# Kernel optimization log

Measured on AMD Instinct MI355X. Metric: run time of the kernel, lower is better.

## Reference

```python
import jax, jax.numpy as jnp
import numpy as np

B, L, V, D, H = 4096, 32, 50000, 300, 6
HD = D // H  # 50


def setup_inputs() -> dict:
    key = jax.random.key(0)
    ks = jax.random.split(key, 9)
    s = 0.02
    return {
        "title": jax.random.randint(ks[0], (B, L), 0, V),
        "emb": jax.random.normal(ks[1], (V, D), dtype=jnp.float32) * s,
        "pos_emb": jax.random.normal(ks[2], (512, D), dtype=jnp.float32) * s,
        "Wq": jax.random.normal(ks[3], (D, D), dtype=jnp.float32) * s,
        "bq": jnp.zeros((D,), jnp.float32),
        "Wk": jax.random.normal(ks[4], (D, D), dtype=jnp.float32) * s,
        "bk": jnp.zeros((D,), jnp.float32),
        "Wv": jax.random.normal(ks[5], (D, D), dtype=jnp.float32) * s,
        "bv": jnp.zeros((D,), jnp.float32),
        "Wo": jax.random.normal(ks[6], (D, D), dtype=jnp.float32) * s,
        "bo": jnp.zeros((D,), jnp.float32),
        "Va": jax.random.normal(ks[7], (D, D), dtype=jnp.float32) * s,
        "ba": jnp.zeros((D,), jnp.float32),
        "qw": jax.random.normal(ks[8], (D, 1), dtype=jnp.float32) * s,
    }


def reference(title, emb, pos_emb, Wq, bq, Wk, bk, Wv, bv, Wo, bo, Va, ba, qw):
    b, l = title.shape
    # word embedding + positional embedding
    x = emb[title] + pos_emb[:l][None, :, :]  # [B, L, D]

    def heads(y):  # [B, L, D] -> [B, H, L, HD]
        return y.reshape(b, l, H, HD).transpose(0, 2, 1, 3)

    # manual multi-head self-attention (mask is all-ones -> no masking effect)
    q = heads(x @ Wq.T + bq) / jnp.sqrt(jnp.float32(HD))
    k = heads(x @ Wk.T + bk)
    v = heads(x @ Wv.T + bv)
    scores = jnp.einsum("bhqd,bhkd->bhqk", q, k)  # [B, H, L, L]
    w = jax.nn.softmax(scores, axis=-1)  # dropout is identity in eval
    ctx = jnp.einsum("bhqk,bhkd->bhqd", w, v)
    ctx = ctx.transpose(0, 2, 1, 3).reshape(b, l, D)
    ctx = ctx @ Wo.T + bo  # [B, L, D]

    # additive attention pooling
    t = jnp.tanh(ctx @ Va.T + ba)          # [B, L, D]
    a = (t @ qw)[..., 0]                    # [B, L]
    alpha = jax.nn.softmax(a, axis=1)       # [B, L]
    out = jnp.einsum("bs,bsd->bd", alpha, ctx)  # [B, D]
    return out
```

## Files before the change

### kernel.cpp

```cpp
#include <hip/hip_runtime.h>
#include <math.h>

typedef _Float16 f16;
typedef _Float16 half8 __attribute__((ext_vector_type(8)));
typedef _Float16 half4 __attribute__((ext_vector_type(4)));
typedef float float4v __attribute__((ext_vector_type(4)));

#define MFMA16(a, b, c) __builtin_amdgcn_mfma_f32_16x16x32_f16((a), (b), (c), 0, 0, 0)


#define WQKV_OFF 0u
#define BQKV_OFF 655360u
#define WO_OFF   659456u
#define WVA_OFF  864256u
#define BVA_OFF  1069056u
#define CBAR_OFF 1070336u
#define XF_OFF   3691776u

__global__ void repack1(const float* __restrict__ Wq, const float* __restrict__ Wk,
                        const float* __restrict__ Wv, const float* __restrict__ Wo,
                        const float* __restrict__ bq, const float* __restrict__ bk,
                        const float* __restrict__ bv,
                        f16* __restrict__ wqkvF, f16* __restrict__ wo16F,
                        float* __restrict__ bqkv) {
    int idx = blockIdx.x * 256 + threadIdx.x;
    const float rs = 0.14142135623730951f;
    if (idx < 327680) {
        int ntile = idx / 5120, rem = idx - ntile * 5120;
        int ks = rem / 512, r2 = rem - ks * 512;
        int lane = r2 >> 3, j = r2 & 7;
        int n = ntile * 16 + (lane & 15);
        int k = ks * 32 + (lane >> 4) * 8 + j;
        int g = n / 320, r = n - g * 320;
        float v = 0.f;
        if (r < 300 && k < 300) {
            if (g == 0) v = Wq[r * 300 + k] * rs;
            else if (g == 1) v = Wk[r * 300 + k];
            else if (g == 2) v = Wv[r * 300 + k];
        }
        wqkvF[idx] = (f16)v;
    } else if (idx < 430080) {
        int t = idx - 327680;
        int ntile = t / 5120, rem = t - ntile * 5120;
        int ks = rem / 512, r2 = rem - ks * 512;
        int lane = r2 >> 3, j = r2 & 7;
        int n = ntile * 16 + (lane & 15);
        int k = ks * 32 + (lane >> 4) * 8 + j;
        wo16F[t] = (f16)((n < 300 && k < 300) ? Wo[n * 300 + k] : 0.f);
    } else if (idx < 431104) {
        int n = idx - 430080;
        int g = n / 320, r = n - g * 320;
        float v = 0.f;
        if (r < 300) {
            if (g == 0) v = bq[r] * rs;
            else if (g == 1) v = bk[r];
            else if (g == 2) v = bv[r];
        }
        bqkv[n] = v;
    }
}

__global__ void repack2(const float* __restrict__ Va, const float* __restrict__ Wo,
                        f16* __restrict__ wvaF) {
    int bt = blockIdx.x;
    int mt = bt / 20, nt = bt % 20;
    int lane = threadIdx.x & 63;
    int lr = lane & 15, quad = lane >> 4;
    float4v acc = {0.f, 0.f, 0.f, 0.f};
    int m = mt * 16 + lr;
    int nn = nt * 16 + lr;
    for (int ks = 0; ks < 10; ++ks) {
        int c = ks * 32 + quad * 8;
        half8 af, bf;
#pragma unroll
        for (int j = 0; j < 8; ++j) {
            int cc = c + j;
            af[j] = (f16)((m < 300 && cc < 300) ? Va[m * 300 + cc] : 0.f);
            bf[j] = (f16)((nn < 300 && cc < 300) ? Wo[cc * 300 + nn] : 0.f);
        }
        acc = MFMA16(af, bf, acc);
    }
#pragma unroll
    for (int r = 0; r < 4; ++r) {
        int row = mt * 16 + quad * 4 + r;
        int col = nt * 16 + lr;
        int addr = ((row >> 4) * 10 + (col >> 5)) * 512 +
                   (((col >> 3) & 3) * 16 + (row & 15)) * 8 + (col & 7);
        wvaF[addr] = (f16)acc[r];
    }
}

__global__ void repack3(const float* __restrict__ Va, const float* __restrict__ bo,
                        const float* __restrict__ ba, float* __restrict__ bva) {
    int j = threadIdx.x;
    float s = 0.f;
    if (j < 300) {
        for (int k = 0; k < 300; ++k) s += Va[j * 300 + k] * bo[k];
        s += ba[j];
    }
    bva[j] = s;
}

__global__ void gather_kernel(const int* __restrict__ title, const float* __restrict__ emb,
                              const float* __restrict__ pos, f16* __restrict__ xF) {
    int c = blockIdx.x * 256 + threadIdx.x;
    int fragblk = c >> 6, lane = c & 63;
    int item = fragblk / 20, rem = fragblk - item * 20;
    int mt = rem / 10, ks = rem - mt * 10;
    int lr = lane & 15, quad = lane >> 4;
    int row = item * 32 + mt * 16 + lr;
    int col = ks * 32 + quad * 8;
    int t = title[row];
    int l = row & 31;
    half8 h;
    if (col + 8 <= 300) {
        float4v e0 = *(const float4v*)&emb[t * 300 + col];
        float4v e1 = *(const float4v*)&emb[t * 300 + col + 4];
        float4v p0 = *(const float4v*)&pos[l * 300 + col];
        float4v p1 = *(const float4v*)&pos[l * 300 + col + 4];
#pragma unroll
        for (int j = 0; j < 4; ++j) { h[j] = (f16)(e0[j] + p0[j]); h[4 + j] = (f16)(e1[j] + p1[j]); }
    } else {
#pragma unroll
        for (int j = 0; j < 8; ++j) {
            int cc = col + j;
            h[j] = (f16)((cc < 300) ? emb[t * 300 + cc] + pos[l * 300 + cc] : 0.f);
        }
    }
    *(half8*)&xF[c * 8] = h;
}

__global__ __launch_bounds__(1024, 4) void qkvattn_kernel(
    const f16* __restrict__ xF, const f16* __restrict__ wqkvF,
    const float* __restrict__ bqkv, const f16* __restrict__ wvaF,
    const float* __restrict__ bva, const float* __restrict__ qw,
    f16* __restrict__ cbar) {
    __shared__ __align__(16) f16 qL[12 * 32 * 72];
    __shared__ __align__(16) f16 kL[12 * 32 * 72];
    __shared__ __align__(16) f16 vT[12 * 64 * 32];
    __shared__ float aL[64];
    __shared__ float alpha[64];
    const int ib = blockIdx.x, tid = threadIdx.x;
    const int w = tid >> 6, lane = tid & 63, lr = lane & 15, quad = lane >> 4;
    const float4v vz = {0.f, 0.f, 0.f, 0.f};

    for (int i = tid; i < 13824; i += 1024) { ((int*)qL)[i] = 0; ((int*)kL)[i] = 0; }
    for (int i = tid; i < 12288; i += 1024) ((int*)vT)[i] = 0;
    if (tid < 64) aL[tid] = 0.f;
    __syncthreads();

    {
        float4v acc[4][4];
#pragma unroll
        for (int mt = 0; mt < 4; ++mt)
#pragma unroll
            for (int j = 0; j < 4; ++j) acc[mt][j] = vz;
        for (int ks = 0; ks < 10; ++ks) {
            half8 a[4];
#pragma unroll
            for (int mt = 0; mt < 4; ++mt)
                a[mt] = *(const half8*)&xF[(((ib * 4 + mt) * 10 + ks) * 64 + lane) * 8];
#pragma unroll
            for (int j = 0; j < 4; ++j) {
                half8 bf = *(const half8*)&wqkvF[((((w * 4 + j) * 10) + ks) * 64 + lane) * 8];
#pragma unroll
                for (int mt = 0; mt < 4; ++mt) acc[mt][j] = MFMA16(a[mt], bf, acc[mt][j]);
            }
        }
#pragma unroll
        for (int j = 0; j < 4; ++j) {
            int tile = w * 4 + j;
            int wi = tile / 20;
            int n = tile * 16 + lr;
            int cc = n - wi * 320;
            float bb = (wi < 3) ? bqkv[n] : 0.f;
            int h = cc / 50, d = cc - h * 50;
            if (wi < 3 && cc < 300) {
                if (wi == 2) {
#pragma unroll
                    for (int mt = 0; mt < 4; ++mt) {
                        int hh = (mt >> 1) * 6 + h;
                        int row0 = (mt & 1) * 16 + quad * 4;
                        half4 pk;
#pragma unroll
                        for (int r = 0; r < 4; ++r) pk[r] = (f16)(acc[mt][j][r] + bb);
                        *(half4*)&vT[(hh * 64 + d) * 32 + row0] = pk;
                    }
                } else {
                    f16* dst = (wi == 0) ? qL : kL;
#pragma unroll
                    for (int mt = 0; mt < 4; ++mt) {
                        int hh = (mt >> 1) * 6 + h;
#pragma unroll
                        for (int r = 0; r < 4; ++r) {
                            int row = (mt & 1) * 16 + quad * 4 + r;
                            dst[(hh * 32 + row) * 72 + d] = (f16)(acc[mt][j][r] + bb);
                        }
                    }
                }
            }
        }
    }
    __syncthreads();

    const int hh = w;
    if (w < 12) {
        float4v s00 = vz, s01 = vz, s10 = vz, s11 = vz;
#pragma unroll
        for (int ks = 0; ks < 2; ++ks) {
            int c = ks * 32 + quad * 8;
            half8 aq0 = *(const half8*)&qL[(hh * 32 + lr) * 72 + c];
            half8 aq1 = *(const half8*)&qL[(hh * 32 + 16 + lr) * 72 + c];
            half8 bk0 = *(const half8*)&kL[(hh * 32 + lr) * 72 + c];
            half8 bk1 = *(const half8*)&kL[(hh * 32 + 16 + lr) * 72 + c];
            s00 = MFMA16(aq0, bk0, s00);
            s01 = MFMA16(aq0, bk1, s01);
            s10 = MFMA16(aq1, bk0, s10);
            s11 = MFMA16(aq1, bk1, s11);
        }
        f16* ph = qL + hh * 32 * 72;
#pragma unroll
        for (int mt = 0; mt < 2; ++mt) {
            float4v sv0 = mt ? s10 : s00;
            float4v sv1 = mt ? s11 : s01;
#pragma unroll
            for (int r = 0; r < 4; ++r) {
                float v0 = sv0[r], v1 = sv1[r];
                float m = fmaxf(v0, v1);
#pragma unroll
                for (int off = 1; off < 16; off <<= 1) m = fmaxf(m, __shfl_xor(m, off, 64));
                float e0 = expf(v0 - m), e1 = expf(v1 - m);
                float ss = e0 + e1;
#pragma unroll
                for (int off = 1; off < 16; off <<= 1) ss += __shfl_xor(ss, off, 64);
                float inv = 1.0f / ss;
                int row = mt * 16 + quad * 4 + r;
                ph[row * 40 + lr] = (f16)(e0 * inv);
                ph[row * 40 + 16 + lr] = (f16)(e1 * inv);
            }
        }
    }
    __syncthreads();

    f16* scratch = kL;
    for (int i = tid; i < 64 * 28; i += 1024) {
        int row = i / 28, cc = 300 + (i - row * 28);
        scratch[row * 328 + cc] = (f16)0.f;
    }
    if (w < 12) {
        int il = hh / 6, h = hh - il * 6;
        f16* ph = qL + hh * 32 * 72;
        half8 aw0 = *(const half8*)&ph[lr * 40 + quad * 8];
        half8 aw1 = *(const half8*)&ph[(16 + lr) * 40 + quad * 8];
        float4v c0[4], c1[4];
#pragma unroll
        for (int nt = 0; nt < 4; ++nt) { c0[nt] = vz; c1[nt] = vz; }
#pragma unroll
        for (int nt = 0; nt < 4; ++nt) {
            half8 bvf = *(const half8*)&vT[(hh * 64 + nt * 16 + lr) * 32 + quad * 8];
            c0[nt] = MFMA16(aw0, bvf, c0[nt]);
            c1[nt] = MFMA16(aw1, bvf, c1[nt]);
        }
#pragma unroll
        for (int mt = 0; mt < 2; ++mt)
#pragma unroll
            for (int nt = 0; nt < 4; ++nt)
#pragma unroll
                for (int r = 0; r < 4; ++r) {
                    int d = nt * 16 + lr;
                    if (d < 50) {
                        int row = il * 32 + mt * 16 + quad * 4 + r;
                        float4v cv = mt ? c1[nt] : c0[nt];
                        scratch[row * 328 + h * 50 + d] = (f16)cv[r];
                    }
                }
    }
    __syncthreads();

    {
        const int mtile = w >> 2, nsub = w & 3;
        float4v vacc[5];
#pragma unroll
        for (int i = 0; i < 5; ++i) vacc[i] = vz;
        const int arow = (mtile * 16 + lr) * 328;
        for (int ks = 0; ks < 10; ++ks) {
            half8 a = *(const half8*)&scratch[arow + ks * 32 + quad * 8];
#pragma unroll
            for (int i = 0; i < 5; ++i) {
                half8 bf = *(const half8*)&wvaF[((((nsub * 5 + i) * 10) + ks) * 64 + lane) * 8];
                vacc[i] = MFMA16(a, bf, vacc[i]);
            }
        }
        float ps[4] = {0.f, 0.f, 0.f, 0.f};
#pragma unroll
        for (int i = 0; i < 5; ++i) {
            int n = (nsub * 5 + i) * 16 + lr;
            float bb = bva[n];
            float qq = (n < 300) ? qw[n] : 0.f;
#pragma unroll
            for (int r = 0; r < 4; ++r) ps[r] += tanhf(vacc[i][r] + bb) * qq;
        }
#pragma unroll
        for (int r = 0; r < 4; ++r)
#pragma unroll
            for (int off = 1; off < 16; off <<= 1) ps[r] += __shfl_xor(ps[r], off, 64);
        if (lr == 0) {
#pragma unroll
            for (int r = 0; r < 4; ++r) atomicAdd(&aL[mtile * 16 + quad * 4 + r], ps[r]);
        }
    }
    __syncthreads();

    if (w == 0) {
        float av = aL[lane];
        float m = av;
#pragma unroll
        for (int off = 1; off < 32; off <<= 1) m = fmaxf(m, __shfl_xor(m, off, 32));
        float e = expf(av - m);
        float ss = e;
#pragma unroll
        for (int off = 1; off < 32; off <<= 1) ss += __shfl_xor(ss, off, 32);
        alpha[lane] = e / ss;
    }
    __syncthreads();

    if (tid < 640) {
        int it = tid / 320, d = tid - it * 320;
        float acc = 0.f;
#pragma unroll
        for (int l = 0; l < 32; ++l)
            acc += alpha[it * 32 + l] * (float)scratch[(it * 32 + l) * 328 + d];
        cbar[ib * 640 + tid] = (f16)acc;
    }
}

__global__ __launch_bounds__(512) void out_kernel(
    const f16* __restrict__ cbar, const f16* __restrict__ wo16F,
    const float* __restrict__ bo, float* __restrict__ out) {
    __shared__ __align__(16) f16 cA[32 * 328];
    const int mb = blockIdx.x, tid = threadIdx.x;
    const int w = tid >> 6, lane = tid & 63, lr = lane & 15, quad = lane >> 4;
    const int mh = w >> 2, nsub = w & 3;
    for (int i = tid; i < 1280; i += 512) {
        int row = i / 40, g = i - row * 40;
        *(half8*)&cA[row * 328 + g * 8] = *(const half8*)&cbar[(mb * 32 + row) * 320 + g * 8];
    }
    __syncthreads();
    const float4v vz = {0.f, 0.f, 0.f, 0.f};
    float4v acc[5];
#pragma unroll
    for (int i = 0; i < 5; ++i) acc[i] = vz;
    for (int ks = 0; ks < 10; ++ks) {
        half8 a = *(const half8*)&cA[(mh * 16 + lr) * 328 + ks * 32 + quad * 8];
#pragma unroll
        for (int i = 0; i < 5; ++i) {
            half8 bf = *(const half8*)&wo16F[((((nsub * 5 + i) * 10) + ks) * 64 + lane) * 8];
            acc[i] = MFMA16(a, bf, acc[i]);
        }
    }
#pragma unroll
    for (int i = 0; i < 5; ++i) {
        int n = (nsub * 5 + i) * 16 + lr;
        if (n < 300) {
            float bb = bo[n];
#pragma unroll
            for (int r = 0; r < 4; ++r)
                out[(mb * 32 + mh * 16 + quad * 4 + r) * 300 + n] = acc[i][r] + bb;
        }
    }
}

extern "C" void kernel_launch(void* const* d_in, const int* in_sizes, int n_in,
                              void* d_out, int out_size, void* d_ws, size_t ws_size,
                              hipStream_t stream) {
    const int* title = (const int*)d_in[0];
    const float* emb = (const float*)d_in[1];
    const float* pos = (const float*)d_in[2];
    const float* Wq = (const float*)d_in[3];
    const float* bq = (const float*)d_in[4];
    const float* Wk = (const float*)d_in[5];
    const float* bk = (const float*)d_in[6];
    const float* Wv = (const float*)d_in[7];
    const float* bv = (const float*)d_in[8];
    const float* Wo = (const float*)d_in[9];
    const float* bo = (const float*)d_in[10];
    const float* Va = (const float*)d_in[11];
    const float* ba = (const float*)d_in[12];
    const float* qw = (const float*)d_in[13];
    char* ws = (char*)d_ws;
    float* out = (float*)d_out;

    f16* wqkvF = (f16*)(ws + WQKV_OFF);
    float* bqkv = (float*)(ws + BQKV_OFF);
    f16* wo16F = (f16*)(ws + WO_OFF);
    f16* wvaF = (f16*)(ws + WVA_OFF);
    float* bva = (float*)(ws + BVA_OFF);
    f16* cbar = (f16*)(ws + CBAR_OFF);
    f16* xF = (f16*)(ws + XF_OFF);

    repack1<<<1684, 256, 0, stream>>>(Wq, Wk, Wv, Wo, bq, bk, bv, wqkvF, wo16F, bqkv);
    repack2<<<400, 64, 0, stream>>>(Va, Wo, wvaF);
    repack3<<<1, 320, 0, stream>>>(Va, bo, ba, bva);
    gather_kernel<<<20480, 256, 0, stream>>>(title, emb, pos, xF);
    qkvattn_kernel<<<2048, 1024, 0, stream>>>(xF, wqkvF, bqkv, wvaF, bva, qw, cbar);
    out_kernel<<<128, 512, 0, stream>>>(cbar, wo16F, bo, out);
}
```

Before: 435.2 us.

## Process one sequence per 512-thread block with swizzled V layout and fast exp/tanh

Each qkvattn block now handles one sequence with 8 waves instead of two sequences with 16 waves, which halves LDS use per block and doubles the grid size. Each wave now covers 8 QKV output tiles across 2 M-tiles instead of 4 tiles across 4 M-tiles. The V-transpose LDS layout gets an XOR swizzle to cut bank conflicts, zero-initialisation uses 16-byte stores, and expf/tanhf are replaced with __expf and an exp-based tanh. Waves 6-7 sit idle in the attention phase, and the fast math slightly lowers accuracy.

```diff
diff --git a/kernel.cpp b/kernel.cpp
--- a/kernel.cpp
+++ b/kernel.cpp
@@ -5,6 +5,7 @@
 typedef _Float16 half8 __attribute__((ext_vector_type(8)));
 typedef _Float16 half4 __attribute__((ext_vector_type(4)));
 typedef float float4v __attribute__((ext_vector_type(4)));
+typedef int int4v __attribute__((ext_vector_type(4)));
 
 #define MFMA16(a, b, c) __builtin_amdgcn_mfma_f32_16x16x32_f16((a), (b), (c), 0, 0, 0)
 
@@ -16,6 +17,11 @@
 #define BVA_OFF  1069056u
 #define CBAR_OFF 1070336u
 #define XF_OFF   3691776u
+
+__device__ __forceinline__ float fast_tanh(float x) {
+    float e = __expf(2.f * x);
+    return 1.f - 2.f / (e + 1.f);
+}
 
 __global__ void repack1(const float* __restrict__ Wq, const float* __restrict__ Wk,
                         const float* __restrict__ Wv, const float* __restrict__ Wo,
@@ -130,73 +136,79 @@
     *(half8*)&xF[c * 8] = h;
 }
 
-__global__ __launch_bounds__(1024, 4) void qkvattn_kernel(
+__global__ __launch_bounds__(512, 4) void qkvattn_kernel(
     const f16* __restrict__ xF, const f16* __restrict__ wqkvF,
     const float* __restrict__ bqkv, const f16* __restrict__ wvaF,
     const float* __restrict__ bva, const float* __restrict__ qw,
     f16* __restrict__ cbar) {
-    __shared__ __align__(16) f16 qL[12 * 32 * 72];
-    __shared__ __align__(16) f16 kL[12 * 32 * 72];
-    __shared__ __align__(16) f16 vT[12 * 64 * 32];
-    __shared__ float aL[64];
-    __shared__ float alpha[64];
+    __shared__ __align__(16) f16 qL[6 * 32 * 72];
+    __shared__ __align__(16) f16 kL[6 * 32 * 72];
+    __shared__ __align__(16) f16 vT[6 * 64 * 32];
+    __shared__ float aL[32];
+    __shared__ float alpha[32];
     const int ib = blockIdx.x, tid = threadIdx.x;
     const int w = tid >> 6, lane = tid & 63, lr = lane & 15, quad = lane >> 4;
     const float4v vz = {0.f, 0.f, 0.f, 0.f};
-
-    for (int i = tid; i < 13824; i += 1024) { ((int*)qL)[i] = 0; ((int*)kL)[i] = 0; }
-    for (int i = tid; i < 12288; i += 1024) ((int*)vT)[i] = 0;
-    if (tid < 64) aL[tid] = 0.f;
-    __syncthreads();
+    const int4v z4 = {0, 0, 0, 0};
 
     {
-        float4v acc[4][4];
-#pragma unroll
-        for (int mt = 0; mt < 4; ++mt)
-#pragma unroll
-            for (int j = 0; j < 4; ++j) acc[mt][j] = vz;
+        int4v* q4 = (int4v*)qL;
+        int4v* k4 = (int4v*)kL;
+        int4v* v4 = (int4v*)vT;
+        for (int i = tid; i < 1728; i += 512) { q4[i] = z4; k4[i] = z4; }
+        for (int i = tid; i < 1536; i += 512) v4[i] = z4;
+        if (tid < 32) aL[tid] = 0.f;
+    }
+    __syncthreads();
+
+    {
+        float4v acc[2][8];
+#pragma unroll
+        for (int mt = 0; mt < 2; ++mt)
+#pragma unroll
+            for (int j = 0; j < 8; ++j) acc[mt][j] = vz;
         for (int ks = 0; ks < 10; ++ks) {
-            half8 a[4];
-#pragma unroll
-            for (int mt = 0; mt < 4; ++mt)
-                a[mt] = *(const half8*)&xF[(((ib * 4 + mt) * 10 + ks) * 64 + lane) * 8];
-#pragma unroll
-            for (int j = 0; j < 4; ++j) {
-                half8 bf = *(const half8*)&wqkvF[((((w * 4 + j) * 10) + ks) * 64 + lane) * 8];
-#pragma unroll
-                for (int mt = 0; mt < 4; ++mt) acc[mt][j] = MFMA16(a[mt], bf, acc[mt][j]);
+            half8 a0 = *(const half8*)&xF[(((ib * 2 + 0) * 10 + ks) * 64 + lane) * 8];
+            half8 a1 = *(const half8*)&xF[(((ib * 2 + 1) * 10 + ks) * 64 + lane) * 8];
+#pragma unroll
+            for (int j = 0; j < 8; ++j) {
+                int tile = w * 8 + j;
+                if (tile < 60) {
+                    half8 bf = *(const half8*)&wqkvF[((tile * 10 + ks) * 64 + lane) * 8];
+                    acc[0][j] = MFMA16(a0, bf, acc[0][j]);
+                    acc[1][j] = MFMA16(a1, bf, acc[1][j]);
+                }
             }
         }
 #pragma unroll
-        for (int j = 0; j < 4; ++j) {
-            int tile = w * 4 + j;
+        for (int j = 0; j < 8; ++j) {
+            int tile = w * 8 + j;
             int wi = tile / 20;
             int n = tile * 16 + lr;
             int cc = n - wi * 320;
-            float bb = (wi < 3) ? bqkv[n] : 0.f;
-            int h = cc / 50, d = cc - h * 50;
             if (wi < 3 && cc < 300) {
+                float bb = bqkv[n];
+                int h = cc / 50, d = cc - h * 50;
                 if (wi == 2) {
 #pragma unroll
-                    for (int mt = 0; mt < 4; ++mt) {
-                        int hh = (mt >> 1) * 6 + h;
-                        int row0 = (mt & 1) * 16 + quad * 4;
+                    for (int mt = 0; mt < 2; ++mt) {
+                        int row0 = mt * 16 + quad * 4;
                         half4 pk;
 #pragma unroll
                         for (int r = 0; r < 4; ++r) pk[r] = (f16)(acc[mt][j][r] + bb);
-                        *(half4*)&vT[(hh * 64 + d) * 32 + row0] = pk;
+                        int idx = (h * 64 + d) * 32 + row0;
+                        int byt = (idx * 2) ^ (((d >> 2) & 3) << 4);
+                        *(half4*)((char*)vT + byt) = pk;
                     }
                 } else {
                     f16* dst = (wi == 0) ? qL : kL;
 #pragma unroll
-                    for (int mt = 0; mt < 4; ++mt) {
-                        int hh = (mt >> 1) * 6 + h;
+                    for (int mt = 0; mt < 2; ++mt)
 #pragma unroll
                         for (int r = 0; r < 4; ++r) {
-                            int row = (mt & 1) * 16 + quad * 4 + r;
-                            dst[(hh * 32 + row) * 72 + d] = (f16)(acc[mt][j][r] + bb);
+                            int row = mt * 16 + quad * 4 + r;
+                            dst[(h * 32 + row) * 72 + d] = (f16)(acc[mt][j][r] + bb);
                         }
-                    }
                 }
             }
         }
@@ -204,7 +216,7 @@
     __syncthreads();
 
     const int hh = w;
-    if (w < 12) {
+    if (w < 6) {
         float4v s00 = vz, s01 = vz, s10 = vz, s11 = vz;
 #pragma unroll
         for (int ks = 0; ks < 2; ++ks) {
@@ -229,7 +241,7 @@
                 float m = fmaxf(v0, v1);
 #pragma unroll
                 for (int off = 1; off < 16; off <<= 1) m = fmaxf(m, __shfl_xor(m, off, 64));
-                float e0 = expf(v0 - m), e1 = expf(v1 - m);
+                float e0 = __expf(v0 - m), e1 = __expf(v1 - m);
                 float ss = e0 + e1;
 #pragma unroll
                 for (int off = 1; off < 16; off <<= 1) ss += __shfl_xor(ss, off, 64);
@@ -243,12 +255,12 @@
     __syncthreads();
 
     f16* scratch = kL;
-    for (int i = tid; i < 64 * 28; i += 1024) {
+    for (int i = tid; i < 32 * 28; i += 512) {
         int row = i / 28, cc = 300 + (i - row * 28);
         scratch[row * 328 + cc] = (f16)0.f;
     }
-    if (w < 12) {
-        int il = hh / 6, h = hh - il * 6;
+    if (w < 6) {
+        int h = hh;
         f16* ph = qL + hh * 32 * 72;
         half8 aw0 = *(const half8*)&ph[lr * 40 + quad * 8];
         half8 aw1 = *(const half8*)&ph[(16 + lr) * 40 + quad * 8];
@@ -257,7 +269,10 @@
         for (int nt = 0; nt < 4; ++nt) { c0[nt] = vz; c1[nt] = vz; }
 #pragma unroll
         for (int nt = 0; nt < 4; ++nt) {
-            half8 bvf = *(const half8*)&vT[(hh * 64 + nt * 16 + lr) * 32 + quad * 8];
+            int rIdx = nt * 16 + lr;
+            int idx = (hh * 64 + rIdx) * 32 + quad * 8;
+            int byt = (idx * 2) ^ (((rIdx >> 2) & 3) << 4);
+            half8 bvf = *(const half8*)((const char*)vT + byt);
             c0[nt] = MFMA16(aw0, bvf, c0[nt]);
             c1[nt] = MFMA16(aw1, bvf, c1[nt]);
         }
@@ -269,7 +284,7 @@
                 for (int r = 0; r < 4; ++r) {
                     int d = nt * 16 + lr;
                     if (d < 50) {
-                        int row = il * 32 + mt * 16 + quad * 4 + r;
+                        int row = mt * 16 + quad * 4 + r;
                         float4v cv = mt ? c1[nt] : c0[nt];
                         scratch[row * 328 + h * 50 + d] = (f16)cv[r];
                     }
@@ -298,7 +313,7 @@
             float bb = bva[n];
             float qq = (n < 300) ? qw[n] : 0.f;
 #pragma unroll
-            for (int r = 0; r < 4; ++r) ps[r] += tanhf(vacc[i][r] + bb) * qq;
+            for (int r = 0; r < 4; ++r) ps[r] += fast_tanh(vacc[i][r] + bb) * qq;
         }
 #pragma unroll
         for (int r = 0; r < 4; ++r)
@@ -311,12 +326,12 @@
     }
     __syncthreads();
 
-    if (w == 0) {
+    if (w == 0 && lane < 32) {
         float av = aL[lane];
         float m = av;
 #pragma unroll
         for (int off = 1; off < 32; off <<= 1) m = fmaxf(m, __shfl_xor(m, off, 32));
-        float e = expf(av - m);
+        float e = __expf(av - m);
         float ss = e;
 #pragma unroll
         for (int off = 1; off < 32; off <<= 1) ss += __shfl_xor(ss, off, 32);
@@ -324,13 +339,13 @@
     }
     __syncthreads();
 
-    if (tid < 640) {
-        int it = tid / 320, d = tid - it * 320;
+    if (tid < 320) {
+        int d = tid;
         float acc = 0.f;
 #pragma unroll
         for (int l = 0; l < 32; ++l)
-            acc += alpha[it * 32 + l] * (float)scratch[(it * 32 + l) * 328 + d];
-        cbar[ib * 640 + tid] = (f16)acc;
+            acc += alpha[l] * (float)scratch[l * 328 + d];
+        cbar[ib * 320 + d] = (f16)acc;
     }
 }
 
@@ -402,6 +417,6 @@
     repack2<<<400, 64, 0, stream>>>(Va, Wo, wvaF);
     repack3<<<1, 320, 0, stream>>>(Va, bo, ba, bva);
     gather_kernel<<<20480, 256, 0, stream>>>(title, emb, pos, xF);
-    qkvattn_kernel<<<2048, 1024, 0, stream>>>(xF, wqkvF, bqkv, wvaF, bva, qw, cbar);
+    qkvattn_kernel<<<4096, 512, 0, stream>>>(xF, wqkvF, bqkv, wvaF, bva, qw, cbar);
     out_kernel<<<128, 512, 0, stream>>>(cbar, wo16F, bo, out);
 }
```

Measured after the change: 448.7 us. 1.03x slower.
